# Kernel optimization log

Measured on AMD Instinct MI355X. Metric: run time of the kernel, lower is better.

## Reference

```python
import jax, jax.numpy as jnp
import numpy as np

NUM_VERTEX = 1448
C = 256


def _decode(latent, eye_labels, left_mu, left_delta, right_mu, right_delta):
    # latent: [B, C, H, W] -> global average pool -> [B, C]
    lat = jnp.mean(latent, axis=(-2, -1))
    # batched decode against both eye models, select per-sample by eye label
    left = lat @ left_delta.T + left_mu[:, 0]    # [B, 3*N]
    right = lat @ right_delta.T + right_mu[:, 0]  # [B, 3*N]
    pts = jnp.where(eye_labels[:, None] == 1, right, left)
    return pts.reshape(lat.shape[0], NUM_VERTEX, 3)  # [B, N, 3]


def _cdist(a, b):
    # Euclidean distance via the norm trick; a,b: [B, N, 3]
    a2 = jnp.sum(a * a, axis=-1)  # [B, N]
    b2 = jnp.sum(b * b, axis=-1)  # [B, M]
    d2 = a2[:, :, None] + b2[:, None, :] - 2.0 * jnp.einsum('bnd,bmd->bnm', a, b)
    return jnp.sqrt(jnp.maximum(d2, 1e-12))


def setup_inputs() -> dict:
    key = jax.random.key(0)
    ks = jax.random.split(key, 8)
    B, H, W = 64, 8, 8
    inputs = jax.random.normal(ks[0], (B, C, H, W), dtype=jnp.float32)
    targets = jax.random.normal(ks[1], (B, C, H, W), dtype=jnp.float32)
    eye_labels = jax.random.randint(ks[2], (B,), 0, 2)
    left_mu = jax.random.normal(ks[3], (3 * NUM_VERTEX, 1), dtype=jnp.float32)
    left_delta = jax.random.normal(ks[4], (3 * NUM_VERTEX, C), dtype=jnp.float32) * 0.1
    right_mu = jax.random.normal(ks[5], (3 * NUM_VERTEX, 1), dtype=jnp.float32)
    right_delta = jax.random.normal(ks[6], (3 * NUM_VERTEX, C), dtype=jnp.float32) * 0.1
    return {"inputs": inputs, "targets": targets, "eye_labels": eye_labels,
            "left_mu": left_mu, "left_delta": left_delta,
            "right_mu": right_mu, "right_delta": right_delta}


def reference(inputs, targets, eye_labels, left_mu, left_delta, right_mu, right_delta):
    pts_in = _decode(inputs, eye_labels, left_mu, left_delta, right_mu, right_delta)
    pts_tg = _decode(targets, eye_labels, left_mu, left_delta, right_mu, right_delta)
    d = _cdist(pts_in, pts_tg)  # [B, N, N]
    dist_1 = jnp.mean(jnp.min(d, axis=-1))
    dist_2 = jnp.mean(jnp.min(d, axis=-2))
    return dist_1 + dist_2
```

## Files before the change

### kernel.cpp

```cpp
#include <hip/hip_runtime.h>

#define NV 1448
#define JD 4344
#define CC 256
#define BB 64
#define QQ 128
#define QCOLS 362
#define NROW (2 * BB * NV)

typedef __bf16 bf16x8 __attribute__((ext_vector_type(8)));
typedef float  f32x4  __attribute__((ext_vector_type(4)));

__device__ __forceinline__ unsigned f2bf(float f) {
    unsigned u = __float_as_uint(f);
    return (u + 0x7FFFu + ((u >> 16) & 1u)) >> 16;
}

__global__ __launch_bounds__(256) void pool_kernel(const float* __restrict__ inp,
                                                   const float* __restrict__ tgt,
                                                   unsigned short* __restrict__ latQb,
                                                   unsigned long long* __restrict__ acc) {
    int gid  = blockIdx.x * 256 + threadIdx.x;
    if (gid == 0) { acc[0] = 0ull; acc[1] = 0ull; }
    int lane = gid & 15;
    int row  = gid >> 4;
    if (row >= 2 * BB * CC) return;
    int t  = row >> 14;
    int bc = row & 16383;
    const float* src = (t ? tgt : inp) + (size_t)bc * 64;
    float4 v = reinterpret_cast<const float4*>(src)[lane];
    float s = (v.x + v.y) + (v.z + v.w);
    s += __shfl_xor(s, 1);
    s += __shfl_xor(s, 2);
    s += __shfl_xor(s, 4);
    s += __shfl_xor(s, 8);
    if (lane == 0) {
        int b = bc >> 8, c = bc & 255;
        latQb[(size_t)(t * 64 + b) * CC + c] = (unsigned short)f2bf(s * (1.0f / 64.0f));
    }
}

__global__ __launch_bounds__(256) void decode_kernel(const unsigned short* __restrict__ latQb,
                                                     const float* __restrict__ muL,
                                                     const float* __restrict__ deltaL,
                                                     const float* __restrict__ muR,
                                                     const float* __restrict__ deltaR,
                                                     const int* __restrict__ labels,
                                                     float* __restrict__ pts3) {
    const int jt   = blockIdx.x;
    const int side = blockIdx.y;
    const int qq   = blockIdx.z;
    const float* __restrict__ delta = side ? deltaR : deltaL;
    const float* __restrict__ mu    = side ? muR : muL;
    const int jb = jt * 64;
    const int q0 = qq * 32;
    const int tid  = threadIdx.x;
    const int w    = tid >> 6;
    const int lane = tid & 63;

    __shared__ unsigned short dB[64 * 264];
    __shared__ unsigned short lB[32 * 264];

#pragma unroll
    for (int i = 0; i < 16; ++i) {
        int idx = i * 256 + tid;
        int row = idx >> 6;
        int ch  = idx & 63;
        int j   = jb + row;
        unsigned u0 = 0, u1 = 0;
        if (j < JD) {
            float4 v = *reinterpret_cast<const float4*>(delta + (size_t)j * CC + ch * 4);
            u0 = f2bf(v.x) | (f2bf(v.y) << 16);
            u1 = f2bf(v.z) | (f2bf(v.w) << 16);
        }
        *reinterpret_cast<uint2*>(&dB[row * 264 + ch * 4]) = make_uint2(u0, u1);
    }
#pragma unroll
    for (int i = 0; i < 4; ++i) {
        int idx = i * 256 + tid;
        int row = idx >> 5;
        int ch  = idx & 31;
        *reinterpret_cast<uint4*>(&lB[row * 264 + ch * 8]) =
            *reinterpret_cast<const uint4*>(latQb + (size_t)(q0 + row) * CC + ch * 8);
    }
    __syncthreads();

    const int col  = lane & 15;
    const int kgrp = lane >> 4;
    bf16x8 bfr[8];
#pragma unroll
    for (int ks = 0; ks < 8; ++ks)
        bfr[ks] = *reinterpret_cast<const bf16x8*>(&dB[(w * 16 + col) * 264 + ks * 32 + kgrp * 8]);

    int j = jb + w * 16 + col;
    float muv = (j < JD) ? mu[j] : 0.f;

#pragma unroll
    for (int mt = 0; mt < 2; ++mt) {
        f32x4 acc = {0.f, 0.f, 0.f, 0.f};
#pragma unroll
        for (int ks = 0; ks < 8; ++ks) {
            bf16x8 a = *reinterpret_cast<const bf16x8*>(&lB[(mt * 16 + col) * 264 + ks * 32 + kgrp * 8]);
            acc = __builtin_amdgcn_mfma_f32_16x16x32_bf16(a, bfr[ks], acc, 0, 0, 0);
        }
        if (j < JD) {
#pragma unroll
            for (int r = 0; r < 4; ++r) {
                int q = q0 + mt * 16 + kgrp * 4 + r;
                if (labels[q & 63] == side)
                    pts3[(size_t)q * JD + j] = acc[r] + muv;
            }
        }
    }
}

__global__ __launch_bounds__(256) void chamfer_kernel(const float* __restrict__ pts3,
                                                      float* __restrict__ pmin) {
    const int chunk = blockIdx.x;
    const int b     = blockIdx.y;
    const int dir   = blockIdx.z >> 2;
    const int q     = blockIdx.z & 3;
    const int qa = dir * BB + b;
    const int qb = (1 - dir) * BB + b;
    const float* __restrict__ A3 = pts3 + (size_t)qa * JD;
    const float* __restrict__ B3 = pts3 + (size_t)qb * JD + q * (QCOLS * 3);

    __shared__ float4 Bs[QCOLS];
    const int tid = threadIdx.x;
    for (int i = tid; i < QCOLS; i += 256) {
        float x = B3[3 * i], y = B3[3 * i + 1], z = B3[3 * i + 2];
        Bs[i] = make_float4(-2.f * x, -2.f * y, -2.f * z, fmaf(x, x, fmaf(y, y, z * z)));
    }
    __syncthreads();

    int r0 = chunk * 512 + tid;
    int r1 = r0 + 256;
    float a0x = 0.f, a0y = 0.f, a0z = 0.f, a0w = 0.f;
    float a1x = 0.f, a1y = 0.f, a1z = 0.f, a1w = 0.f;
    if (r0 < NV) {
        a0x = A3[3 * r0]; a0y = A3[3 * r0 + 1]; a0z = A3[3 * r0 + 2];
        a0w = fmaf(a0x, a0x, fmaf(a0y, a0y, a0z * a0z));
    }
    if (r1 < NV) {
        a1x = A3[3 * r1]; a1y = A3[3 * r1 + 1]; a1z = A3[3 * r1 + 2];
        a1w = fmaf(a1x, a1x, fmaf(a1y, a1y, a1z * a1z));
    }
    float m0 = 1e30f, m1 = 1e30f;

#pragma unroll 2
    for (int m = 0; m < QCOLS; m += 2) {
        float4 b0 = Bs[m];
        float4 b1 = Bs[m + 1];
        float d00 = fmaf(b0.x, a0x, fmaf(b0.y, a0y, fmaf(b0.z, a0z, b0.w)));
        float d01 = fmaf(b1.x, a0x, fmaf(b1.y, a0y, fmaf(b1.z, a0z, b1.w)));
        asm("v_min3_f32 %0, %0, %1, %2" : "+v"(m0) : "v"(d00), "v"(d01));
        float d10 = fmaf(b0.x, a1x, fmaf(b0.y, a1y, fmaf(b0.z, a1z, b0.w)));
        float d11 = fmaf(b1.x, a1x, fmaf(b1.y, a1y, fmaf(b1.z, a1z, b1.w)));
        asm("v_min3_f32 %0, %0, %1, %2" : "+v"(m1) : "v"(d10), "v"(d11));
    }

    size_t base = (size_t)q * NROW + (size_t)qa * NV;
    if (r0 < NV) pmin[base + r0] = m0 + a0w;
    if (r1 < NV) pmin[base + r1] = m1 + a1w;
}

__global__ __launch_bounds__(256) void combine_kernel(const float* __restrict__ pmin,
                                                      unsigned long long* __restrict__ acc,
                                                      float* __restrict__ out) {
    const int base = blockIdx.x * 724;
    const int tid  = threadIdx.x;
    float s = 0.f;
#pragma unroll
    for (int it = 0; it < 3; ++it) {
        int idx = it * 256 + tid;
        if (idx < 724) {
            int g = base + idx;
            float v = fminf(fminf(pmin[g], pmin[g + NROW]),
                            fminf(pmin[g + 2 * NROW], pmin[g + 3 * NROW]));
            s += sqrtf(fmaxf(v, 1e-12f));
        }
    }
    s += __shfl_xor(s, 1);
    s += __shfl_xor(s, 2);
    s += __shfl_xor(s, 4);
    s += __shfl_xor(s, 8);
    s += __shfl_xor(s, 16);
    s += __shfl_xor(s, 32);
    __shared__ float wsum[4];
    if ((tid & 63) == 0) wsum[tid >> 6] = s;
    __syncthreads();
    if (tid == 0) {
        float bs = wsum[0] + wsum[1] + wsum[2] + wsum[3];
        unsigned long long qv = (unsigned long long)((double)bs * 16777216.0);
        atomicAdd(acc, qv);
        __threadfence();
        unsigned long long done = atomicAdd(acc + 1, 1ull);
        if (done == 255) {
            __threadfence();
            unsigned long long total = atomicAdd(acc, 0ull);
            out[0] = (float)((double)total * (0x1p-24 / (64.0 * 1448.0)));
        }
    }
}

extern "C" void kernel_launch(void* const* d_in, const int* in_sizes, int n_in,
                              void* d_out, int out_size, void* d_ws, size_t ws_size,
                              hipStream_t stream) {
    const float* inp    = (const float*)d_in[0];
    const float* tgt    = (const float*)d_in[1];
    const int*   labels = (const int*)d_in[2];
    const float* muL    = (const float*)d_in[3];
    const float* deltaL = (const float*)d_in[4];
    const float* muR    = (const float*)d_in[5];
    const float* deltaR = (const float*)d_in[6];
    float* out = (float*)d_out;

    char* ws = (char*)d_ws;
    unsigned short* latQb = (unsigned short*)ws;
    float* pts3 = (float*)(ws + 65536);
    float* pmin = (float*)(ws + 65536 + 2224128);
    unsigned long long* acc = (unsigned long long*)(ws + 65536 + 2224128 + 2965504);

    hipLaunchKernelGGL(pool_kernel, dim3(2048), dim3(256), 0, stream, inp, tgt, latQb, acc);
    hipLaunchKernelGGL(decode_kernel, dim3(68, 2, 4), dim3(256), 0, stream,
                       latQb, muL, deltaL, muR, deltaR, labels, pts3);
    hipLaunchKernelGGL(chamfer_kernel, dim3(3, 64, 8), dim3(256), 0, stream,
                       pts3, pmin);
    hipLaunchKernelGGL(combine_kernel, dim3(256), dim3(256), 0, stream, pmin, acc, out);
}
```

Before: 51.91 us.

## Compute chamfer distances with fp16 split-precision MFMA and single-pass bidirectional minima

Replaces the scalar FMA chamfer loop with MFMA matrix products. A new pack kernel encodes each point as a 16-element fp16 vector holding hi/lo split coordinates and norms, so that one 16x16x32 MFMA yields the squared distances directly. Each block computes the distance tile once and reduces both row minima and column minima from it, which removes the second directional pass and the four partial-min arrays. Padded rows carry a large norm so they never win a minimum. The cost is an extra pack kernel and its workspace, and the hi/lo fp16 split may lose some precision compared with the fp32 version.

After: 82.08 us. 58.1% more time.

```diff
diff --git a/kernel.cpp b/kernel.cpp
--- a/kernel.cpp
+++ b/kernel.cpp
@@ -5,16 +5,22 @@
 #define CC 256
 #define BB 64
 #define QQ 128
-#define QCOLS 362
-#define NROW (2 * BB * NV)
-
-typedef __bf16 bf16x8 __attribute__((ext_vector_type(8)));
-typedef float  f32x4  __attribute__((ext_vector_type(4)));
+#define NPAD 1456
+#define NTC 91
+#define NSLICE 13
+#define PADV 60000.0f
+
+typedef __bf16    bf16x8 __attribute__((ext_vector_type(8)));
+typedef _Float16  f16x8  __attribute__((ext_vector_type(8)));
+typedef float     f32x4  __attribute__((ext_vector_type(4)));
 
 __device__ __forceinline__ unsigned f2bf(float f) {
     unsigned u = __float_as_uint(f);
     return (u + 0x7FFFu + ((u >> 16) & 1u)) >> 16;
 }
+union HU { _Float16 h; unsigned short u; };
+__device__ __forceinline__ unsigned short f2h(float f) { HU t; t.h = (_Float16)f; return t.u; }
+__device__ __forceinline__ float h2f(unsigned short u) { HU t; t.u = u; return (float)t.h; }
 
 __global__ __launch_bounds__(256) void pool_kernel(const float* __restrict__ inp,
                                                    const float* __restrict__ tgt,
@@ -114,70 +120,136 @@
     }
 }
 
-__global__ __launch_bounds__(256) void chamfer_kernel(const float* __restrict__ pts3,
-                                                      float* __restrict__ pmin) {
-    const int chunk = blockIdx.x;
+__global__ __launch_bounds__(256) void pack_kernel(const float* __restrict__ pts3,
+                                                   unsigned short* __restrict__ Apack,
+                                                   unsigned short* __restrict__ Bpack) {
+    int idx = blockIdx.x * 256 + threadIdx.x;
+    if (idx >= QQ * NPAD) return;
+    int q = idx / NPAD;
+    int n = idx - q * NPAD;
+    float x = 0.f, y = 0.f, z = 0.f;
+    bool real = n < NV;
+    if (real) {
+        const float* p = pts3 + (size_t)q * JD + n * 3;
+        x = p[0]; y = p[1]; z = p[2];
+    }
+    float p2 = fmaf(x, x, fmaf(y, y, z * z));
+    if (!real) p2 = PADV;
+    unsigned short p2h = f2h(p2);
+    unsigned short p2l = f2h(p2 - h2f(p2h));
+    unsigned short one = f2h(1.0f);
+    unsigned short out[16];
+    if (q < BB) {
+        unsigned short ahx = f2h(-2.f * x), ahy = f2h(-2.f * y), ahz = f2h(-2.f * z);
+        unsigned short alx = f2h(-2.f * x - h2f(ahx));
+        unsigned short aly = f2h(-2.f * y - h2f(ahy));
+        unsigned short alz = f2h(-2.f * z - h2f(ahz));
+        out[0] = ahx; out[1] = ahx; out[2] = alx;
+        out[3] = ahy; out[4] = ahy; out[5] = aly;
+        out[6] = ahz; out[7] = ahz; out[8] = alz;
+        out[9] = one; out[10] = one; out[11] = p2h; out[12] = p2l;
+        out[13] = out[14] = out[15] = 0;
+        uint4* dst = reinterpret_cast<uint4*>(Apack + ((size_t)q * NPAD + n) * 16);
+        dst[0] = *reinterpret_cast<uint4*>(&out[0]);
+        dst[1] = *reinterpret_cast<uint4*>(&out[8]);
+    } else {
+        unsigned short bhx = f2h(x), bhy = f2h(y), bhz = f2h(z);
+        unsigned short blx = f2h(x - h2f(bhx));
+        unsigned short bly = f2h(y - h2f(bhy));
+        unsigned short blz = f2h(z - h2f(bhz));
+        out[0] = bhx; out[1] = blx; out[2] = bhx;
+        out[3] = bhy; out[4] = bly; out[5] = bhy;
+        out[6] = bhz; out[7] = blz; out[8] = bhz;
+        out[9] = p2h; out[10] = p2l; out[11] = one; out[12] = one;
+        out[13] = out[14] = out[15] = 0;
+        uint4* dst = reinterpret_cast<uint4*>(Bpack + ((size_t)(q - BB) * NPAD + n) * 16);
+        dst[0] = *reinterpret_cast<uint4*>(&out[0]);
+        dst[1] = *reinterpret_cast<uint4*>(&out[8]);
+    }
+}
+
+__global__ __launch_bounds__(256) void chamfer_kernel(const unsigned short* __restrict__ Apack,
+                                                      const unsigned short* __restrict__ Bpack,
+                                                      float* __restrict__ cmin,
+                                                      unsigned long long* __restrict__ acc) {
+    const int slice = blockIdx.x;
     const int b     = blockIdx.y;
-    const int dir   = blockIdx.z >> 2;
-    const int q     = blockIdx.z & 3;
-    const int qa = dir * BB + b;
-    const int qb = (1 - dir) * BB + b;
-    const float* __restrict__ A3 = pts3 + (size_t)qa * JD;
-    const float* __restrict__ B3 = pts3 + (size_t)qb * JD + q * (QCOLS * 3);
-
-    __shared__ float4 Bs[QCOLS];
-    const int tid = threadIdx.x;
-    for (int i = tid; i < QCOLS; i += 256) {
-        float x = B3[3 * i], y = B3[3 * i + 1], z = B3[3 * i + 2];
-        Bs[i] = make_float4(-2.f * x, -2.f * y, -2.f * z, fmaf(x, x, fmaf(y, y, z * z)));
-    }
-    __syncthreads();
-
-    int r0 = chunk * 512 + tid;
-    int r1 = r0 + 256;
-    float a0x = 0.f, a0y = 0.f, a0z = 0.f, a0w = 0.f;
-    float a1x = 0.f, a1y = 0.f, a1z = 0.f, a1w = 0.f;
-    if (r0 < NV) {
-        a0x = A3[3 * r0]; a0y = A3[3 * r0 + 1]; a0z = A3[3 * r0 + 2];
-        a0w = fmaf(a0x, a0x, fmaf(a0y, a0y, a0z * a0z));
-    }
-    if (r1 < NV) {
-        a1x = A3[3 * r1]; a1y = A3[3 * r1 + 1]; a1z = A3[3 * r1 + 2];
-        a1w = fmaf(a1x, a1x, fmaf(a1y, a1y, a1z * a1z));
-    }
-    float m0 = 1e30f, m1 = 1e30f;
-
-#pragma unroll 2
-    for (int m = 0; m < QCOLS; m += 2) {
-        float4 b0 = Bs[m];
-        float4 b1 = Bs[m + 1];
-        float d00 = fmaf(b0.x, a0x, fmaf(b0.y, a0y, fmaf(b0.z, a0z, b0.w)));
-        float d01 = fmaf(b1.x, a0x, fmaf(b1.y, a0y, fmaf(b1.z, a0z, b1.w)));
-        asm("v_min3_f32 %0, %0, %1, %2" : "+v"(m0) : "v"(d00), "v"(d01));
-        float d10 = fmaf(b0.x, a1x, fmaf(b0.y, a1y, fmaf(b0.z, a1z, b0.w)));
-        float d11 = fmaf(b1.x, a1x, fmaf(b1.y, a1y, fmaf(b1.z, a1z, b1.w)));
-        asm("v_min3_f32 %0, %0, %1, %2" : "+v"(m1) : "v"(d10), "v"(d11));
-    }
-
-    size_t base = (size_t)q * NROW + (size_t)qa * NV;
-    if (r0 < NV) pmin[base + r0] = m0 + a0w;
-    if (r1 < NV) pmin[base + r1] = m1 + a1w;
-}
-
-__global__ __launch_bounds__(256) void combine_kernel(const float* __restrict__ pmin,
-                                                      unsigned long long* __restrict__ acc,
-                                                      float* __restrict__ out) {
-    const int base = blockIdx.x * 724;
-    const int tid  = threadIdx.x;
+    const int tid   = threadIdx.x;
+    const int w     = tid >> 6;
+    const int lane  = tid & 63;
+    const int col   = lane & 15;
+    const int kgrp  = lane >> 4;
+    const int half  = kgrp & 1;
+
+    __shared__ unsigned short BsL[NPAD * 16 + 8];
+    __shared__ float rmbuf[4 * 112];
+
+    {
+        const uint4* src = reinterpret_cast<const uint4*>(Bpack + (size_t)b * NPAD * 16);
+        uint4* dst = reinterpret_cast<uint4*>(BsL);
+        for (int i = tid; i < 2912; i += 256) dst[i] = src[i];
+        if (tid == 0) dst[2912] = make_uint4(0, 0, 0, 0);
+    }
+    __syncthreads();
+
+    const char* Ab = (const char*)(Apack + ((size_t)b * NPAD + slice * 112) * 16);
+    f16x8 afr[7];
+#pragma unroll
+    for (int tr = 0; tr < 7; ++tr)
+        afr[tr] = *reinterpret_cast<const f16x8*>(Ab + (tr * 16 + col) * 32 + half * 16);
+
+    float rm[7][4];
+#pragma unroll
+    for (int tr = 0; tr < 7; ++tr)
+#pragma unroll
+        for (int r = 0; r < 4; ++r) rm[tr][r] = 1e30f;
+
+    const int tcs[5] = {0, 23, 46, 69, 91};
+    const char* Bb = (const char*)BsL;
+    const f32x4 zero4 = {0.f, 0.f, 0.f, 0.f};
+
+    for (int tc = tcs[w]; tc < tcs[w + 1]; ++tc) {
+        int daddr = (tc * 16 + col) * 32 + half * 16;
+        int addr  = (kgrp < 2) ? daddr : (NPAD * 32);
+        f16x8 bfrag = *reinterpret_cast<const f16x8*>(Bb + addr);
+        float cmv = 1e30f;
+#pragma unroll
+        for (int tr = 0; tr < 7; ++tr) {
+            f32x4 d = __builtin_amdgcn_mfma_f32_16x16x32_f16(afr[tr], bfrag, zero4, 0, 0, 0);
+            rm[tr][0] = fminf(rm[tr][0], d[0]);
+            rm[tr][1] = fminf(rm[tr][1], d[1]);
+            rm[tr][2] = fminf(rm[tr][2], d[2]);
+            rm[tr][3] = fminf(rm[tr][3], d[3]);
+            float t;
+            asm("v_min3_f32 %0, %1, %2, %3" : "=v"(t) : "v"(d[0]), "v"(d[1]), "v"(d[2]));
+            asm("v_min3_f32 %0, %0, %1, %2" : "+v"(cmv) : "v"(t), "v"(d[3]));
+        }
+        cmv = fminf(cmv, __shfl_xor(cmv, 16));
+        cmv = fminf(cmv, __shfl_xor(cmv, 32));
+        if (lane < 16)
+            cmin[((size_t)slice * BB + b) * NPAD + tc * 16 + lane] = cmv;
+    }
+
+#pragma unroll
+    for (int tr = 0; tr < 7; ++tr)
+#pragma unroll
+        for (int r = 0; r < 4; ++r) {
+            float v = rm[tr][r];
+            v = fminf(v, __shfl_xor(v, 1));
+            v = fminf(v, __shfl_xor(v, 2));
+            v = fminf(v, __shfl_xor(v, 4));
+            v = fminf(v, __shfl_xor(v, 8));
+            if (col == 0) rmbuf[w * 112 + tr * 16 + kgrp * 4 + r] = v;
+        }
+    __syncthreads();
+
     float s = 0.f;
-#pragma unroll
-    for (int it = 0; it < 3; ++it) {
-        int idx = it * 256 + tid;
-        if (idx < 724) {
-            int g = base + idx;
-            float v = fminf(fminf(pmin[g], pmin[g + NROW]),
-                            fminf(pmin[g + 2 * NROW], pmin[g + 3 * NROW]));
-            s += sqrtf(fmaxf(v, 1e-12f));
+    if (tid < 112) {
+        int row = slice * 112 + tid;
+        if (row < NV) {
+            float v = fminf(fminf(rmbuf[tid], rmbuf[112 + tid]),
+                            fminf(rmbuf[224 + tid], rmbuf[336 + tid]));
+            s = sqrtf(fmaxf(v, 1e-12f));
         }
     }
     s += __shfl_xor(s, 1);
@@ -190,12 +262,40 @@
     if ((tid & 63) == 0) wsum[tid >> 6] = s;
     __syncthreads();
     if (tid == 0) {
-        float bs = wsum[0] + wsum[1] + wsum[2] + wsum[3];
-        unsigned long long qv = (unsigned long long)((double)bs * 16777216.0);
-        atomicAdd(acc, qv);
+        float bs = (wsum[0] + wsum[1]) + (wsum[2] + wsum[3]);
+        atomicAdd(acc, (unsigned long long)((double)bs * 16777216.0));
+    }
+}
+
+__global__ __launch_bounds__(256) void combine_kernel(const float* __restrict__ cmin,
+                                                      unsigned long long* __restrict__ acc,
+                                                      float* __restrict__ out) {
+    int idx = blockIdx.x * 256 + threadIdx.x;
+    int b = idx / NPAD;
+    int n = idx - b * NPAD;
+    float s = 0.f;
+    if (n < NV) {
+        float v = 1e30f;
+#pragma unroll
+        for (int sl = 0; sl < NSLICE; ++sl)
+            v = fminf(v, cmin[((size_t)sl * BB + b) * NPAD + n]);
+        s = sqrtf(fmaxf(v, 1e-12f));
+    }
+    s += __shfl_xor(s, 1);
+    s += __shfl_xor(s, 2);
+    s += __shfl_xor(s, 4);
+    s += __shfl_xor(s, 8);
+    s += __shfl_xor(s, 16);
+    s += __shfl_xor(s, 32);
+    __shared__ float wsum[4];
+    if ((threadIdx.x & 63) == 0) wsum[threadIdx.x >> 6] = s;
+    __syncthreads();
+    if (threadIdx.x == 0) {
+        float bs = (wsum[0] + wsum[1]) + (wsum[2] + wsum[3]);
+        atomicAdd(acc, (unsigned long long)((double)bs * 16777216.0));
         __threadfence();
         unsigned long long done = atomicAdd(acc + 1, 1ull);
-        if (done == 255) {
+        if (done == 363) {
             __threadfence();
             unsigned long long total = atomicAdd(acc, 0ull);
             out[0] = (float)((double)total * (0x1p-24 / (64.0 * 1448.0)));
@@ -217,14 +317,17 @@
 
     char* ws = (char*)d_ws;
     unsigned short* latQb = (unsigned short*)ws;
-    float* pts3 = (float*)(ws + 65536);
-    float* pmin = (float*)(ws + 65536 + 2224128);
-    unsigned long long* acc = (unsigned long long*)(ws + 65536 + 2224128 + 2965504);
+    float* pts3           = (float*)(ws + 65536);
+    unsigned short* Apack = (unsigned short*)(ws + 65536 + 2224128);
+    unsigned short* Bpack = (unsigned short*)(ws + 5271552);
+    float* cmin           = (float*)(ws + 8253440);
+    unsigned long long* acc = (unsigned long long*)(ws + 13099008);
 
     hipLaunchKernelGGL(pool_kernel, dim3(2048), dim3(256), 0, stream, inp, tgt, latQb, acc);
     hipLaunchKernelGGL(decode_kernel, dim3(68, 2, 4), dim3(256), 0, stream,
                        latQb, muL, deltaL, muR, deltaR, labels, pts3);
-    hipLaunchKernelGGL(chamfer_kernel, dim3(3, 64, 8), dim3(256), 0, stream,
-                       pts3, pmin);
-    hipLaunchKernelGGL(combine_kernel, dim3(256), dim3(256), 0, stream, pmin, acc, out);
-}
+    hipLaunchKernelGGL(pack_kernel, dim3(728), dim3(256), 0, stream, pts3, Apack, Bpack);
+    hipLaunchKernelGGL(chamfer_kernel, dim3(NSLICE, BB), dim3(256), 0, stream,
+                       Apack, Bpack, cmin, acc);
+    hipLaunchKernelGGL(combine_kernel, dim3(364), dim3(256), 0, stream, cmin, acc, out);
+}
```
